# Optimization experiments

Hardware: AMD Instinct MI355X
Metric: run time of the kernel (lower is better)

Reference implementation:

```python
import jax, jax.numpy as jnp
import numpy as np

N_NODES = 50000
N_EDGES = 800000
F_DIM = 64


def setup_inputs() -> dict:
    key = jax.random.key(0)
    ks = jax.random.split(key, 8)
    idx_i = jax.random.randint(ks[0], (N_EDGES,), 0, N_NODES)
    idx_j = jax.random.randint(ks[1], (N_EDGES,), 0, N_NODES)
    px = jax.random.normal(ks[2], (N_NODES, 3, F_DIM), dtype=jnp.float32)
    diff = jax.random.normal(ks[3], (N_EDGES, 3, 1), dtype=jnp.float32)
    s = 1.0 / np.sqrt(F_DIM)
    W_pp = jax.random.normal(ks[4], (F_DIM, F_DIM), dtype=jnp.float32) * s
    W_i = jax.random.normal(ks[5], (F_DIM, F_DIM), dtype=jnp.float32) * s
    W_j = jax.random.normal(ks[6], (F_DIM, F_DIM), dtype=jnp.float32) * s
    W_ii = jax.random.normal(ks[7], (F_DIM, F_DIM), dtype=jnp.float32) * s
    return {"idx_i": idx_i, "idx_j": idx_j, "px": px, "diff": diff,
            "W_pp": W_pp, "W_i": W_i, "W_j": W_j, "W_ii": W_ii}


def reference(idx_i, idx_j, px, diff, W_pp, W_i, W_j, W_ii):
    # PPLayer: bias-free linear on feature dim. px: [N, 3, F]
    px1 = jnp.einsum('nvf,gf->nvg', px, W_pp)
    # PIXLayer: gather endpoints, two bias-free linears, sum. [E, 3, F]
    ix = (jnp.einsum('evf,gf->evg', px1[idx_i], W_i)
          + jnp.einsum('evf,gf->evg', px1[idx_j], W_j))
    # ScaleLayer: elementwise scale by per-edge direction. diff: [E, 3, 1]
    ix = ix * diff
    # IILayer: bias-free linear on edge messages
    ix = jnp.einsum('evf,gf->evg', ix, W_ii)
    # IPLayer: scatter_add back to nodes along dim 0
    px_out = jax.ops.segment_sum(ix, idx_i, num_segments=N_NODES)
    return (px_out, ix)
```

## Files before the change

kernel.cpp:

```cpp
#include <hip/hip_runtime.h>

#define N_NODES 50000
#define N_EDGES 800000
#define F 64
#define NROWS (N_NODES * 3)
#define NPX (N_NODES * 3 * F)

typedef float floatx4 __attribute__((ext_vector_type(4)));

__device__ __forceinline__ unsigned short f2bf(float f) {
  unsigned int u = __float_as_uint(f);
  return (unsigned short)((u + 0x7FFFu + ((u >> 16) & 1u)) >> 16);
}
__device__ __forceinline__ float bf2f(unsigned short h) {
  return __uint_as_float(((unsigned int)h) << 16);
}

__global__ __launch_bounds__(256) void mm64_pair(
    const float* __restrict__ A0, const float* __restrict__ B0, float* __restrict__ O0,
    const float* __restrict__ A1, const float* __restrict__ B1, float* __restrict__ O1) {
  const float* A = (blockIdx.x == 0) ? A0 : A1;
  const float* B = (blockIdx.x == 0) ? B0 : B1;
  float* O = (blockIdx.x == 0) ? O0 : O1;
  __shared__ float As[64][65];
  __shared__ float Bs[64][65];
  int t = threadIdx.x;
  for (int k = 0; k < 16; ++k) {
    int idx = t + 256 * k;
    As[idx >> 6][idx & 63] = A[idx];
    Bs[idx >> 6][idx & 63] = B[idx];
  }
  __syncthreads();
  int g = t >> 2, f0 = (t & 3) * 16;
  float acc[16];
  #pragma unroll
  for (int j = 0; j < 16; ++j) acc[j] = 0.f;
  for (int k = 0; k < 64; ++k) {
    float a = As[g][k];
    #pragma unroll
    for (int j = 0; j < 16; ++j) acc[j] += a * Bs[k][f0 + j];
  }
  for (int j = 0; j < 16; ++j) O[g * 64 + f0 + j] = acc[j];
}

__global__ __launch_bounds__(256) void node_mm(
    const float* __restrict__ px, const float* __restrict__ Bi,
    const float* __restrict__ Bj, float* __restrict__ yi,
    unsigned short* __restrict__ yjb) {
  __shared__ float pxs[64][68];
  __shared__ float Bs[128][68];
  int t = threadIdx.x;
  int r0 = blockIdx.x * 64;
  #pragma unroll
  for (int k = 0; k < 8; ++k) {
    int idx = t + 256 * k;
    int row = idx >> 4, c4 = (idx & 15) * 4;
    const float* src = (row < 64) ? (Bi + row * 64 + c4) : (Bj + (row - 64) * 64 + c4);
    *(float4*)&Bs[row][c4] = *(const float4*)src;
  }
  #pragma unroll
  for (int k = 0; k < 4; ++k) {
    int idx = t + 256 * k;
    int lr = idx >> 4, c4 = (idx & 15) * 4;
    float4 v = make_float4(0.f, 0.f, 0.f, 0.f);
    if (r0 + lr < NROWS) v = *(const float4*)(px + (size_t)(r0 + lr) * 64 + c4);
    *(float4*)&pxs[lr][c4] = v;
  }
  __syncthreads();
  int q = t & 31;
  int rg = t >> 5;
  float acc[8][4];
  #pragma unroll
  for (int r = 0; r < 8; ++r)
    #pragma unroll
    for (int j = 0; j < 4; ++j) acc[r][j] = 0.f;
  #pragma unroll 4
  for (int fc = 0; fc < 16; ++fc) {
    float4 b[4];
    #pragma unroll
    for (int j = 0; j < 4; ++j) b[j] = *(const float4*)&Bs[4 * q + j][fc * 4];
    #pragma unroll
    for (int r = 0; r < 8; ++r) {
      float4 p = *(const float4*)&pxs[rg * 8 + r][fc * 4];
      #pragma unroll
      for (int j = 0; j < 4; ++j)
        acc[r][j] += p.x * b[j].x + p.y * b[j].y + p.z * b[j].z + p.w * b[j].w;
    }
  }
  #pragma unroll
  for (int r = 0; r < 8; ++r) {
    int grow = r0 + rg * 8 + r;
    if (grow >= NROWS) continue;
    if (q < 16) {
      float4 v = make_float4(acc[r][0], acc[r][1], acc[r][2], acc[r][3]);
      *(float4*)(yi + (size_t)grow * 64 + q * 4) = v;
    } else {
      ushort4 h;
      h.x = f2bf(acc[r][0]); h.y = f2bf(acc[r][1]);
      h.z = f2bf(acc[r][2]); h.w = f2bf(acc[r][3]);
      *(ushort4*)(yjb + (size_t)grow * 64 + (q - 16) * 4) = h;
    }
  }
}

__global__ __launch_bounds__(256) void hist_kernel(
    const int* __restrict__ idx_i, int* __restrict__ cnt) {
  int e = blockIdx.x * 256 + threadIdx.x;
  if (e < N_EDGES) atomicAdd(&cnt[idx_i[e]], 1);
}

__global__ __launch_bounds__(1024) void scan_kernel(
    const int* __restrict__ cnt, int* __restrict__ offs, int* __restrict__ cursor) {
  __shared__ int wsum[16];
  __shared__ int s_carry;
  int t = threadIdx.x, w = t >> 6, l = t & 63;
  if (t == 0) { s_carry = 0; offs[0] = 0; }
  __syncthreads();
  for (int base = 0; base < N_NODES; base += 8192) {
    int i0 = base + t * 8;
    int x[8];
    if (i0 + 7 < N_NODES) {
      int4 a = *(const int4*)(cnt + i0);
      int4 b = *(const int4*)(cnt + i0 + 4);
      x[0] = a.x; x[1] = a.y; x[2] = a.z; x[3] = a.w;
      x[4] = b.x; x[5] = b.y; x[6] = b.z; x[7] = b.w;
    } else {
      #pragma unroll
      for (int k = 0; k < 8; ++k) x[k] = (i0 + k < N_NODES) ? cnt[i0 + k] : 0;
    }
    int incl[8];
    int p = 0;
    #pragma unroll
    for (int k = 0; k < 8; ++k) { p += x[k]; incl[k] = p; }
    int tsum = p;
    int ts = tsum;
    #pragma unroll
    for (int off = 1; off < 64; off <<= 1) {
      int y = __shfl_up(ts, off, 64);
      if (l >= off) ts += y;
    }
    if (l == 63) wsum[w] = ts;
    __syncthreads();
    if (t < 16) {
      int ws_ = wsum[t];
      int si = ws_;
      #pragma unroll
      for (int off = 1; off < 16; off <<= 1) {
        int y = __shfl_up(si, off, 16);
        if (t >= off) si += y;
      }
      wsum[t] = si - ws_;
    }
    __syncthreads();
    int basev = s_carry + wsum[w] + (ts - tsum);
    #pragma unroll
    for (int k = 0; k < 8; ++k) {
      int i = i0 + k;
      if (i < N_NODES) {
        int it = basev + incl[k];
        offs[i + 1] = it;
        cursor[i] = it - x[k];
      }
    }
    __syncthreads();
    if (t == 1023) s_carry = basev + tsum;
    __syncthreads();
  }
}

__global__ __launch_bounds__(256) void scatter_kernel(
    const int* __restrict__ idx_i, const int* __restrict__ idx_j,
    const float* __restrict__ diff, int* __restrict__ cursor,
    int* __restrict__ perm, int* __restrict__ pnj, float* __restrict__ pdiff) {
  int e = blockIdx.x * 256 + threadIdx.x;
  if (e < N_EDGES) {
    int pos = atomicAdd(&cursor[idx_i[e]], 1);
    perm[pos] = e;
    pnj[pos] = idx_j[e];
    pdiff[pos * 3 + 0] = diff[e * 3 + 0];
    pdiff[pos * 3 + 1] = diff[e * 3 + 1];
    pdiff[pos * 3 + 2] = diff[e * 3 + 2];
  }
}

__global__ __launch_bounds__(192) void node_edge_kernel(
    const int* __restrict__ offs, const int* __restrict__ perm,
    const int* __restrict__ pnj, const float* __restrict__ pdiff,
    const float* __restrict__ yi, const unsigned short* __restrict__ yjb,
    float* __restrict__ ix_out, float* __restrict__ px_out) {
  int n = blockIdx.x;
  int v = threadIdx.x >> 6;
  int lane = threadIdx.x & 63;
  int s = lane >> 4;
  int fq = (lane & 15) * 4;
  int start = offs[n], end = offs[n + 1];
  const float4 yiv = *(const float4*)(yi + ((size_t)n * 3 + v) * 64 + fq);
  float4 acc = make_float4(0.f, 0.f, 0.f, 0.f);
  float sum_d = 0.f;

  for (int p = start + s; p < end; p += 4) {
    int e   = perm[p];
    int nj  = pnj[p];
    float d = pdiff[p * 3 + v];
    const ushort4 yw = *(const ushort4*)(yjb + ((size_t)nj * 3 + v) * 64 + fq);
    float4 yjv = make_float4(bf2f(yw.x), bf2f(yw.y), bf2f(yw.z), bf2f(yw.w));
    acc.x += d * yjv.x; acc.y += d * yjv.y;
    acc.z += d * yjv.z; acc.w += d * yjv.w;
    sum_d += d;
    floatx4 r;
    r.x = d * (yiv.x + yjv.x); r.y = d * (yiv.y + yjv.y);
    r.z = d * (yiv.z + yjv.z); r.w = d * (yiv.w + yjv.w);
    __builtin_nontemporal_store(r, (floatx4*)(ix_out + ((size_t)e * 3 + v) * 64 + fq));
  }
  #pragma unroll
  for (int mm = 16; mm < 64; mm <<= 1) {
    acc.x += __shfl_xor(acc.x, mm, 64);
    acc.y += __shfl_xor(acc.y, mm, 64);
    acc.z += __shfl_xor(acc.z, mm, 64);
    acc.w += __shfl_xor(acc.w, mm, 64);
    sum_d += __shfl_xor(sum_d, mm, 64);
  }
  if (s == 0) {
    float4 o = make_float4(yiv.x * sum_d + acc.x, yiv.y * sum_d + acc.y,
                           yiv.z * sum_d + acc.z, yiv.w * sum_d + acc.w);
    *(float4*)(px_out + ((size_t)n * 3 + v) * 64 + fq) = o;
  }
}

extern "C" void kernel_launch(void* const* d_in, const int* in_sizes, int n_in,
                              void* d_out, int out_size, void* d_ws, size_t ws_size,
                              hipStream_t stream) {
  const int*   idx_i = (const int*)d_in[0];
  const int*   idx_j = (const int*)d_in[1];
  const float* px    = (const float*)d_in[2];
  const float* diff  = (const float*)d_in[3];
  const float* W_pp  = (const float*)d_in[4];
  const float* W_i   = (const float*)d_in[5];
  const float* W_j   = (const float*)d_in[6];
  const float* W_ii  = (const float*)d_in[7];

  float* px_out = (float*)d_out;
  float* ix_out = (float*)d_out + NPX;

  float* ws = (float*)d_ws;
  float* yi = ws;
  unsigned short* yjb = (unsigned short*)(yi + (size_t)NPX);
  float* Ci = (float*)(yjb + (size_t)NPX);
  float* Cj = Ci + 4096;
  float* Bi = Cj + 4096;
  float* Bj = Bi + 4096;
  int* cnt    = (int*)(Bj + 4096);
  int* offs   = cnt + N_NODES;
  int* cursor = offs + N_NODES + 1;
  int* perm   = cursor + N_NODES;
  int* pnj    = perm + N_EDGES;
  float* pdiff = (float*)(pnj + N_EDGES);

  (void)hipMemsetAsync(cnt, 0, N_NODES * sizeof(int), stream);

  mm64_pair<<<2, 256, 0, stream>>>(W_ii, W_i, Ci, W_ii, W_j, Cj);
  mm64_pair<<<2, 256, 0, stream>>>(Ci, W_pp, Bi, Cj, W_pp, Bj);

  node_mm<<<(NROWS + 63) / 64, 256, 0, stream>>>(px, Bi, Bj, yi, yjb);

  hist_kernel<<<(N_EDGES + 255) / 256, 256, 0, stream>>>(idx_i, cnt);
  scan_kernel<<<1, 1024, 0, stream>>>(cnt, offs, cursor);
  scatter_kernel<<<(N_EDGES + 255) / 256, 256, 0, stream>>>(
      idx_i, idx_j, diff, cursor, perm, pnj, pdiff);

  node_edge_kernel<<<N_NODES, 192, 0, stream>>>(offs, perm, pnj, pdiff,
                                                yi, yjb, ix_out, px_out);
}
```

Measured before the change: 320.7 us.

## Fuse weight-chain matmuls, merge histogram into node matmul, widen edge lanes

```diff
diff --git a/kernel.cpp b/kernel.cpp
--- a/kernel.cpp
+++ b/kernel.cpp
@@ -5,8 +5,11 @@
 #define F 64
 #define NROWS (N_NODES * 3)
 #define NPX (N_NODES * 3 * F)
+#define NMM_BLOCKS ((NROWS + 63) / 64)
+#define HIST_BLOCKS ((N_EDGES + 1023) / 1024)
 
 typedef float floatx4 __attribute__((ext_vector_type(4)));
+typedef unsigned short ushortx8 __attribute__((ext_vector_type(8)));
 
 __device__ __forceinline__ unsigned short f2bf(float f) {
   unsigned int u = __float_as_uint(f);
@@ -16,19 +19,21 @@
   return __uint_as_float(((unsigned int)h) << 16);
 }
 
-__global__ __launch_bounds__(256) void mm64_pair(
-    const float* __restrict__ A0, const float* __restrict__ B0, float* __restrict__ O0,
-    const float* __restrict__ A1, const float* __restrict__ B1, float* __restrict__ O1) {
-  const float* A = (blockIdx.x == 0) ? A0 : A1;
-  const float* B = (blockIdx.x == 0) ? B0 : B1;
-  float* O = (blockIdx.x == 0) ? O0 : O1;
+__global__ __launch_bounds__(256) void mm64_chain(
+    const float* __restrict__ W_ii, const float* __restrict__ W_i,
+    const float* __restrict__ W_j, const float* __restrict__ W_pp,
+    float* __restrict__ Bi, float* __restrict__ Bj) {
+  const float* Wx = (blockIdx.x == 0) ? W_i : W_j;
+  float* Out = (blockIdx.x == 0) ? Bi : Bj;
   __shared__ float As[64][65];
   __shared__ float Bs[64][65];
+  __shared__ float Ps[64][65];
   int t = threadIdx.x;
   for (int k = 0; k < 16; ++k) {
     int idx = t + 256 * k;
-    As[idx >> 6][idx & 63] = A[idx];
-    Bs[idx >> 6][idx & 63] = B[idx];
+    As[idx >> 6][idx & 63] = W_ii[idx];
+    Bs[idx >> 6][idx & 63] = Wx[idx];
+    Ps[idx >> 6][idx & 63] = W_pp[idx];
   }
   __syncthreads();
   int g = t >> 2, f0 = (t & 3) * 16;
@@ -40,15 +45,37 @@
     #pragma unroll
     for (int j = 0; j < 16; ++j) acc[j] += a * Bs[k][f0 + j];
   }
-  for (int j = 0; j < 16; ++j) O[g * 64 + f0 + j] = acc[j];
-}
-
-__global__ __launch_bounds__(256) void node_mm(
+  __syncthreads();
+  #pragma unroll
+  for (int j = 0; j < 16; ++j) As[g][f0 + j] = acc[j];
+  __syncthreads();
+  #pragma unroll
+  for (int j = 0; j < 16; ++j) acc[j] = 0.f;
+  for (int k = 0; k < 64; ++k) {
+    float a = As[g][k];
+    #pragma unroll
+    for (int j = 0; j < 16; ++j) acc[j] += a * Ps[k][f0 + j];
+  }
+  for (int j = 0; j < 16; ++j) Out[g * 64 + f0 + j] = acc[j];
+}
+
+__global__ __launch_bounds__(256) void node_mm_hist(
     const float* __restrict__ px, const float* __restrict__ Bi,
     const float* __restrict__ Bj, float* __restrict__ yi,
-    unsigned short* __restrict__ yjb) {
+    unsigned short* __restrict__ yjb,
+    const int* __restrict__ idx_i, int* __restrict__ cnt) {
   __shared__ float pxs[64][68];
   __shared__ float Bs[128][68];
+  if (blockIdx.x >= NMM_BLOCKS) {
+    int b = blockIdx.x - NMM_BLOCKS;
+    int base = b * 1024 + threadIdx.x;
+    #pragma unroll
+    for (int k = 0; k < 4; ++k) {
+      int e = base + k * 256;
+      if (e < N_EDGES) atomicAdd(&cnt[idx_i[e]], 1);
+    }
+    return;
+  }
   int t = threadIdx.x;
   int r0 = blockIdx.x * 64;
   #pragma unroll
@@ -101,12 +128,6 @@
       *(ushort4*)(yjb + (size_t)grow * 64 + (q - 16) * 4) = h;
     }
   }
-}
-
-__global__ __launch_bounds__(256) void hist_kernel(
-    const int* __restrict__ idx_i, int* __restrict__ cnt) {
-  int e = blockIdx.x * 256 + threadIdx.x;
-  if (e < N_EDGES) atomicAdd(&cnt[idx_i[e]], 1);
 }
 
 __global__ __launch_bounds__(1024) void scan_kernel(
@@ -191,39 +212,45 @@
   int n = blockIdx.x;
   int v = threadIdx.x >> 6;
   int lane = threadIdx.x & 63;
-  int s = lane >> 4;
-  int fq = (lane & 15) * 4;
+  int s = lane >> 3;
+  int fo = (lane & 7) * 8;
   int start = offs[n], end = offs[n + 1];
-  const float4 yiv = *(const float4*)(yi + ((size_t)n * 3 + v) * 64 + fq);
-  float4 acc = make_float4(0.f, 0.f, 0.f, 0.f);
-  float sum_d = 0.f;
-
-  for (int p = start + s; p < end; p += 4) {
+  size_t nrow = ((size_t)n * 3 + v) * 64 + fo;
+  const floatx4 yia = __builtin_nontemporal_load((const floatx4*)(yi + nrow));
+  const floatx4 yib = __builtin_nontemporal_load((const floatx4*)(yi + nrow + 4));
+  float yi8[8] = {yia.x, yia.y, yia.z, yia.w, yib.x, yib.y, yib.z, yib.w};
+  float pacc[8];
+  #pragma unroll
+  for (int j = 0; j < 8; ++j) pacc[j] = 0.f;
+
+  for (int p = start + s; p < end; p += 8) {
     int e   = perm[p];
     int nj  = pnj[p];
     float d = pdiff[p * 3 + v];
-    const ushort4 yw = *(const ushort4*)(yjb + ((size_t)nj * 3 + v) * 64 + fq);
-    float4 yjv = make_float4(bf2f(yw.x), bf2f(yw.y), bf2f(yw.z), bf2f(yw.w));
-    acc.x += d * yjv.x; acc.y += d * yjv.y;
-    acc.z += d * yjv.z; acc.w += d * yjv.w;
-    sum_d += d;
-    floatx4 r;
-    r.x = d * (yiv.x + yjv.x); r.y = d * (yiv.y + yjv.y);
-    r.z = d * (yiv.z + yjv.z); r.w = d * (yiv.w + yjv.w);
-    __builtin_nontemporal_store(r, (floatx4*)(ix_out + ((size_t)e * 3 + v) * 64 + fq));
-  }
-  #pragma unroll
-  for (int mm = 16; mm < 64; mm <<= 1) {
-    acc.x += __shfl_xor(acc.x, mm, 64);
-    acc.y += __shfl_xor(acc.y, mm, 64);
-    acc.z += __shfl_xor(acc.z, mm, 64);
-    acc.w += __shfl_xor(acc.w, mm, 64);
-    sum_d += __shfl_xor(sum_d, mm, 64);
+    const ushortx8 yw = *(const ushortx8*)(yjb + ((size_t)nj * 3 + v) * 64 + fo);
+    float r[8];
+    #pragma unroll
+    for (int j = 0; j < 8; ++j) {
+      float yjv = bf2f(yw[j]);
+      r[j] = d * (yi8[j] + yjv);
+      pacc[j] += r[j];
+    }
+    float* dst = ix_out + ((size_t)e * 3 + v) * 64 + fo;
+    floatx4 r0 = {r[0], r[1], r[2], r[3]};
+    floatx4 r1 = {r[4], r[5], r[6], r[7]};
+    __builtin_nontemporal_store(r0, (floatx4*)dst);
+    __builtin_nontemporal_store(r1, (floatx4*)(dst + 4));
+  }
+  #pragma unroll
+  for (int m = 8; m < 64; m <<= 1) {
+    #pragma unroll
+    for (int j = 0; j < 8; ++j) pacc[j] += __shfl_xor(pacc[j], m, 64);
   }
   if (s == 0) {
-    float4 o = make_float4(yiv.x * sum_d + acc.x, yiv.y * sum_d + acc.y,
-                           yiv.z * sum_d + acc.z, yiv.w * sum_d + acc.w);
-    *(float4*)(px_out + ((size_t)n * 3 + v) * 64 + fq) = o;
+    floatx4 o0 = {pacc[0], pacc[1], pacc[2], pacc[3]};
+    floatx4 o1 = {pacc[4], pacc[5], pacc[6], pacc[7]};
+    __builtin_nontemporal_store(o0, (floatx4*)(px_out + nrow));
+    __builtin_nontemporal_store(o1, (floatx4*)(px_out + nrow + 4));
   }
 }
 
@@ -245,9 +272,7 @@
   float* ws = (float*)d_ws;
   float* yi = ws;
   unsigned short* yjb = (unsigned short*)(yi + (size_t)NPX);
-  float* Ci = (float*)(yjb + (size_t)NPX);
-  float* Cj = Ci + 4096;
-  float* Bi = Cj + 4096;
+  float* Bi = (float*)(yjb + (size_t)NPX);
   float* Bj = Bi + 4096;
   int* cnt    = (int*)(Bj + 4096);
   int* offs   = cnt + N_NODES;
@@ -258,12 +283,11 @@
 
   (void)hipMemsetAsync(cnt, 0, N_NODES * sizeof(int), stream);
 
-  mm64_pair<<<2, 256, 0, stream>>>(W_ii, W_i, Ci, W_ii, W_j, Cj);
-  mm64_pair<<<2, 256, 0, stream>>>(Ci, W_pp, Bi, Cj, W_pp, Bj);
-
-  node_mm<<<(NROWS + 63) / 64, 256, 0, stream>>>(px, Bi, Bj, yi, yjb);
-
-  hist_kernel<<<(N_EDGES + 255) / 256, 256, 0, stream>>>(idx_i, cnt);
+  mm64_chain<<<2, 256, 0, stream>>>(W_ii, W_i, W_j, W_pp, Bi, Bj);
+
+  node_mm_hist<<<NMM_BLOCKS + HIST_BLOCKS, 256, 0, stream>>>(
+      px, Bi, Bj, yi, yjb, idx_i, cnt);
+
   scan_kernel<<<1, 1024, 0, stream>>>(cnt, offs, cursor);
   scatter_kernel<<<(N_EDGES + 255) / 256, 256, 0, stream>>>(
       idx_i, idx_j, diff, cursor, perm, pnj, pdiff);
```

Result: slower. 363.3 us (+13.3%).
